# Kernel optimization log

Hardware: AMD Instinct MI355X
Metric: run time of the kernel (lower is better)

## Reference

```python
import jax, jax.numpy as jnp
import numpy as np
import math

B, L, D_MODEL = 4, 2048, 32
H, F = 2, 16  # num_heads, feature_dim (== head_dim)
RD = math.sqrt(F)          # sqrt(input_dim) = 4
R2 = math.sqrt(2.0)
RRD = math.sqrt(RD)        # = 2


def setup_inputs() -> dict:
    key = jax.random.key(0)
    ks = jax.random.split(key, 5)
    s = 1.0 / math.sqrt(D_MODEL)
    return {
        "hidden_states": jax.random.normal(ks[0], (B, L, D_MODEL), jnp.float32),
        "Wq": jax.random.normal(ks[1], (D_MODEL, H * F), jnp.float32) * s,
        "Wk": jax.random.normal(ks[2], (D_MODEL, H * F), jnp.float32) * s,
        "Wv": jax.random.normal(ks[3], (D_MODEL, H * F), jnp.float32) * s,
        "Wo": jax.random.normal(ks[4], (H * F, D_MODEL), jnp.float32) * s,
    }


def _lin_attn(Q, K, V):
    # Q,K,V: [b,h,n,d] with d=f=e=16. Taylor-series linear attention, causal.
    b, h, n, d = Q.shape
    # 2nd-order term
    A2 = jnp.cumsum(jnp.einsum('bhnd,bhnf,bhne->bhndef', K, V, K), axis=2) / (RD * R2)
    Q2 = jnp.einsum('bhnd,bhne->bhnde', Q, Q) / (RD * R2)
    T2 = jnp.einsum('bhnde,bhndef->bhnf', Q2, A2)
    # 1st-order term
    A1 = jnp.cumsum(jnp.einsum('bhnd,bhne->bhnde', K, V), axis=2) / RRD
    T1 = jnp.einsum('bhnd,bhnde->bhne', Q / RRD, A1)
    # 0th-order term
    T0 = jnp.cumsum(V, axis=2)
    # denominators
    K2cs = jnp.cumsum(jnp.einsum('bhnd,bhne->bhnde', K, K), axis=2) / (RD * R2)
    D2 = jnp.einsum('bhnde,bhnde->bhn', Q2, K2cs)
    D1 = jnp.einsum('bhnd,bhnd->bhn', Q, jnp.cumsum(K, axis=2)) / (RRD ** 2)
    D0 = jnp.broadcast_to(jnp.arange(1, n + 1, dtype=Q.dtype), (b, h, n))
    numerator = T0 + T1 + T2
    denominator = D0 + D1 + D2
    return numerator / denominator[..., None]  # [b,h,n,f]


def reference(hidden_states, Wq, Wk, Wv, Wo):
    b, l, _ = hidden_states.shape
    q = (hidden_states @ Wq).reshape(b, l, H, F).transpose(0, 2, 1, 3)
    k = (hidden_states @ Wk).reshape(b, l, H, F).transpose(0, 2, 1, 3)
    v = (hidden_states @ Wv).reshape(b, l, H, F).transpose(0, 2, 1, 3)
    y = _lin_attn(q, k, v)                       # [b,h,l,f]
    y = y.transpose(0, 2, 1, 3).reshape(b, l, H * F)  # b l (h d)
    return y @ Wo
```

## Files before the change

kernel.cpp:

```cpp
#include <hip/hip_runtime.h>

#define L_SEQ 2048
#define NH 2
#define FD 16
#define BH 8
#define NQT 16
#define NSC 16

typedef _Float16 half4f __attribute__((ext_vector_type(4)));
typedef float floatx4 __attribute__((ext_vector_type(4)));

struct FalseT { static constexpr bool value = false; };
struct TrueT  { static constexpr bool value = true;  };

__global__ __launch_bounds__(256) void qkv_proj_kernel(
    const float* __restrict__ hs, const float* __restrict__ Wq,
    const float* __restrict__ Wk, const float* __restrict__ Wv,
    _Float16* __restrict__ q, _Float16* __restrict__ k,
    _Float16* __restrict__ v) {
  __shared__ float sW[3][32][32];
  __shared__ float sH[32][32];
  int tid = threadIdx.x;
  float* swf = &sW[0][0][0];
  for (int i = tid; i < 3072; i += 256)
    swf[i] = (i < 1024) ? Wq[i] : (i < 2048) ? Wk[i - 1024] : Wv[i - 2048];
  int row0 = blockIdx.x * 32;
  int r0 = tid >> 5, c = tid & 31;
  for (int p = 0; p < 4; p++) {
    int r = r0 + p * 8;
    sH[r][c] = hs[(size_t)(row0 + r) * 32 + c];
  }
  __syncthreads();
  int hh = c >> 4, f = c & 15;
  for (int p = 0; p < 4; p++) {
    int r = r0 + p * 8;
    float aq = 0.f, ak = 0.f, av = 0.f;
#pragma unroll
    for (int i = 0; i < 32; i++) {
      float h = sH[r][i];
      aq += h * sW[0][i][c];
      ak += h * sW[1][i][c];
      av += h * sW[2][i][c];
    }
    int row = row0 + r;
    int b = row >> 11, l = row & (L_SEQ - 1);
    size_t idx = (((size_t)(b * NH + hh)) * L_SEQ + l) * FD + f;
    q[idx] = (_Float16)(aq * 0.25f);
    k[idx] = (_Float16)ak;
    v[idx] = (_Float16)av;
  }
}

__global__ __launch_bounds__(256) void attn_partial_kernel(
    const _Float16* __restrict__ q, const _Float16* __restrict__ k,
    const _Float16* __restrict__ v, float* __restrict__ pnum,
    float* __restrict__ pden) {
  __shared__ _Float16 sK[128][24];
  __shared__ _Float16 sVT[16][136];
  int tid = threadIdx.x;
  int bh = blockIdx.y;
  int x = blockIdx.x;
  int qt = 0;
  while ((qt + 1) * (qt + 2) / 2 <= x) qt++;
  int sc = x - qt * (qt + 1) / 2;

  {
    int s = tid >> 1, h = tid & 1;
    const _Float16* kp = k + ((size_t)bh * L_SEQ + sc * 128 + s) * FD + 8 * h;
    const _Float16* vp = v + ((size_t)bh * L_SEQ + sc * 128 + s) * FD + 8 * h;
    uint4 kw = *(const uint4*)kp;
    *(uint4*)&sK[s][8 * h] = kw;
    union { uint4 u; _Float16 e[8]; } vu;
    vu.u = *(const uint4*)vp;
#pragma unroll
    for (int i = 0; i < 8; i++) sVT[8 * h + i][s] = vu.e[i];
  }

  int lane = tid & 63;
  int wid = tid >> 6;
  int lm = lane & 15, lg = lane >> 4;

  half4f qf[2];
  {
    const _Float16* qb = q + ((size_t)bh * L_SEQ + qt * 128 + wid * 32) * FD;
#pragma unroll
    for (int sub = 0; sub < 2; sub++)
      qf[sub] = *(const half4f*)(qb + (sub * 16 + lm) * FD + 4 * lg);
  }
  floatx4 o[2];
  float dn[2];
#pragma unroll
  for (int i = 0; i < 2; i++) {
    o[i] = (floatx4){0.f, 0.f, 0.f, 0.f};
    dn[i] = 0.f;
  }
  int tq[2];
#pragma unroll
  for (int sub = 0; sub < 2; sub++)
    tq[sub] = qt * 128 + wid * 32 + sub * 16 + lm;
  int sb = sc * 128 + 4 * lg;

  __syncthreads();

  auto body = [&](auto mc) {
    constexpr bool MASK = decltype(mc)::value;
#pragma unroll
    for (int st = 0; st < 8; st++) {
      half4f kf = *(const half4f*)&sK[st * 16 + lm][4 * lg];
      half4f vf = *(const half4f*)&sVT[lm][st * 16 + 4 * lg];
#pragma unroll
      for (int sub = 0; sub < 2; sub++) {
        floatx4 sT = __builtin_amdgcn_mfma_f32_16x16x16f16(
            kf, qf[sub], (floatx4){0.f, 0.f, 0.f, 0.f}, 0, 0, 0);
        float wvv[4];
#pragma unroll
        for (int r = 0; r < 4; r++) {
          float a = sT[r];
          float wr = (0.5f * a + 1.f) * a + 1.f;
          if (MASK) wr = (sb + st * 16 + r <= tq[sub]) ? wr : 0.f;
          wvv[r] = wr;
          dn[sub] += wr;
        }
        half4f wf = {(_Float16)wvv[0], (_Float16)wvv[1],
                     (_Float16)wvv[2], (_Float16)wvv[3]};
        o[sub] = __builtin_amdgcn_mfma_f32_16x16x16f16(wf, vf, o[sub], 0, 0, 0);
      }
    }
  };
  if (sc < qt) body(FalseT{}); else body(TrueT{});

#pragma unroll
  for (int sub = 0; sub < 2; sub++) {
    dn[sub] += __shfl_xor(dn[sub], 16, 64);
    dn[sub] += __shfl_xor(dn[sub], 32, 64);
  }

  size_t pb = ((size_t)(bh * NQT + qt) * NSC + sc) * 128;
  float* nb = pnum + (pb + wid * 32) * 16;
#pragma unroll
  for (int sub = 0; sub < 2; sub++)
#pragma unroll
    for (int r = 0; r < 4; r++)
      nb[(sub * 16 + 4 * lg + r) * 16 + lm] = o[sub][r];
  if (lg == 0) {
#pragma unroll
    for (int sub = 0; sub < 2; sub++)
      pden[pb + wid * 32 + sub * 16 + lm] = dn[sub];
  }
}

__global__ __launch_bounds__(256) void reduce_outproj_kernel(
    const float* __restrict__ pnum, const float* __restrict__ pden,
    const float* __restrict__ Wo, float* __restrict__ out) {
  __shared__ float sY[64][33];
  __shared__ float sWo[32][32];
  int tid = threadIdx.x;
  for (int i = tid; i < 1024; i += 256) (&sWo[0][0])[i] = Wo[i];

  int ql = tid >> 2, fq = tid & 3;
  int t = blockIdx.x * 64 + ql;
  int b = blockIdx.y;
  int qt = t >> 7;
  int qloc = t & 127;

  for (int h = 0; h < NH; h++) {
    int bh = b * NH + h;
    size_t tb = ((size_t)(bh * NQT + qt) * NSC) * 128;
    const float* nb = pnum + (tb + qloc) * 16 + fq * 4;
    const float* db = pden + tb + qloc;
    float a0 = 0.f, a1 = 0.f, a2 = 0.f, a3 = 0.f, den = 0.f;
    for (int sc = 0; sc <= qt; sc++) {
      float4 p = *(const float4*)(nb + (size_t)sc * 128 * 16);
      a0 += p.x; a1 += p.y; a2 += p.z; a3 += p.w;
      den += db[(size_t)sc * 128];
    }
    float inv = 1.f / den;
    int cb = h * 16 + fq * 4;
    sY[ql][cb + 0] = a0 * inv;
    sY[ql][cb + 1] = a1 * inv;
    sY[ql][cb + 2] = a2 * inv;
    sY[ql][cb + 3] = a3 * inv;
  }
  __syncthreads();

  int c = tid & 31, r0 = tid >> 5;
  float wo[32];
#pragma unroll
  for (int i = 0; i < 32; i++) wo[i] = sWo[i][c];
#pragma unroll
  for (int p = 0; p < 8; p++) {
    int r = r0 + p * 8;
    float a = 0.f;
#pragma unroll
    for (int i = 0; i < 32; i++) a += sY[r][i] * wo[i];
    out[((size_t)b * L_SEQ + blockIdx.x * 64 + r) * 32 + c] = a;
  }
}

extern "C" void kernel_launch(void* const* d_in, const int* in_sizes, int n_in,
                              void* d_out, int out_size, void* d_ws, size_t ws_size,
                              hipStream_t stream) {
  const float* hs = (const float*)d_in[0];
  const float* Wq = (const float*)d_in[1];
  const float* Wk = (const float*)d_in[2];
  const float* Wv = (const float*)d_in[3];
  const float* Wo = (const float*)d_in[4];
  float* out = (float*)d_out;

  char* wb = (char*)d_ws;
  const size_t PER = (size_t)BH * L_SEQ * FD;
  _Float16* qh = (_Float16*)wb;
  _Float16* kh = qh + PER;
  _Float16* vh = kh + PER;
  float* pnum = (float*)(wb + 3 * PER * sizeof(_Float16));
  float* pden = pnum + (size_t)BH * NQT * NSC * 128 * 16;

  qkv_proj_kernel<<<256, 256, 0, stream>>>(hs, Wq, Wk, Wv, qh, kh, vh);
  attn_partial_kernel<<<dim3(136, BH), 256, 0, stream>>>(qh, kh, vh, pnum, pden);
  reduce_outproj_kernel<<<dim3(32, 4), 256, 0, stream>>>(pnum, pden, Wo, out);
}
```

Baseline: 90.07 us.

## Fuse attention, reduction and output projection into one per-query-tile kernel

Replaces the split-KV partial kernel and the separate reduce/out-projection kernel with a single kernel. Each block owns a 32-query tile for both heads of one batch and loops serially over all causal 128-key chunks, then normalizes and applies Wo in place. This removes the partial numerator/denominator round-trip through global memory and one launch. In exchange, per-block work is serial and unbalanced, the longest tile walks all 16 chunks, and only 256 blocks run, with processing ordered longest-first.

```diff
diff --git a/kernel.cpp b/kernel.cpp
--- a/kernel.cpp
+++ b/kernel.cpp
@@ -4,8 +4,9 @@
 #define NH 2
 #define FD 16
 #define BH 8
-#define NQT 16
-#define NSC 16
+#define QT 32
+#define NT 64
+#define SCW 128
 
 typedef _Float16 half4f __attribute__((ext_vector_type(4)));
 typedef float floatx4 __attribute__((ext_vector_type(4)));
@@ -51,135 +52,86 @@
   }
 }
 
-__global__ __launch_bounds__(256) void attn_partial_kernel(
+__global__ __launch_bounds__(256) void attn_fused_kernel(
     const _Float16* __restrict__ q, const _Float16* __restrict__ k,
-    const _Float16* __restrict__ v, float* __restrict__ pnum,
-    float* __restrict__ pden) {
-  __shared__ _Float16 sK[128][24];
-  __shared__ _Float16 sVT[16][136];
+    const _Float16* __restrict__ v, const float* __restrict__ Wo,
+    float* __restrict__ out) {
+  __shared__ _Float16 sK[NH][128][24];
+  __shared__ _Float16 sVT[NH][16][136];
+  __shared__ float sDen[4][16];
+  __shared__ float sY[QT][33];
+  __shared__ float sWo[32][32];
+
   int tid = threadIdx.x;
-  int bh = blockIdx.y;
-  int x = blockIdx.x;
-  int qt = 0;
-  while ((qt + 1) * (qt + 2) / 2 <= x) qt++;
-  int sc = x - qt * (qt + 1) / 2;
-
-  {
-    int s = tid >> 1, h = tid & 1;
-    const _Float16* kp = k + ((size_t)bh * L_SEQ + sc * 128 + s) * FD + 8 * h;
-    const _Float16* vp = v + ((size_t)bh * L_SEQ + sc * 128 + s) * FD + 8 * h;
-    uint4 kw = *(const uint4*)kp;
-    *(uint4*)&sK[s][8 * h] = kw;
-    union { uint4 u; _Float16 e[8]; } vu;
-    vu.u = *(const uint4*)vp;
-#pragma unroll
-    for (int i = 0; i < 8; i++) sVT[8 * h + i][s] = vu.e[i];
-  }
-
+  int b = blockIdx.y;
+  int t = NT - 1 - (int)blockIdx.x;
   int lane = tid & 63;
   int wid = tid >> 6;
   int lm = lane & 15, lg = lane >> 4;
+  int h = wid >> 1, sub = wid & 1;
+  int bh = b * NH + h;
 
-  half4f qf[2];
-  {
-    const _Float16* qb = q + ((size_t)bh * L_SEQ + qt * 128 + wid * 32) * FD;
-#pragma unroll
-    for (int sub = 0; sub < 2; sub++)
-      qf[sub] = *(const half4f*)(qb + (sub * 16 + lm) * FD + 4 * lg);
-  }
-  floatx4 o[2];
-  float dn[2];
-#pragma unroll
-  for (int i = 0; i < 2; i++) {
-    o[i] = (floatx4){0.f, 0.f, 0.f, 0.f};
-    dn[i] = 0.f;
-  }
-  int tq[2];
-#pragma unroll
-  for (int sub = 0; sub < 2; sub++)
-    tq[sub] = qt * 128 + wid * 32 + sub * 16 + lm;
-  int sb = sc * 128 + 4 * lg;
+  for (int i = tid; i < 1024; i += 256) (&sWo[0][0])[i] = Wo[i];
 
-  __syncthreads();
+  int q0 = t * QT + sub * 16;
+  half4f qf = *(const half4f*)(q + ((size_t)bh * L_SEQ + q0 + lm) * FD + 4 * lg);
 
-  auto body = [&](auto mc) {
+  floatx4 o = (floatx4){0.f, 0.f, 0.f, 0.f};
+  float dn = 0.f;
+  int tq = q0 + lm;
+  int lastc = t >> 2;
+  int ss = tid >> 1, hf = tid & 1;
+
+  auto body = [&](int sc, auto mc) {
     constexpr bool MASK = decltype(mc)::value;
+    int sb = sc * SCW + 4 * lg;
 #pragma unroll
     for (int st = 0; st < 8; st++) {
-      half4f kf = *(const half4f*)&sK[st * 16 + lm][4 * lg];
-      half4f vf = *(const half4f*)&sVT[lm][st * 16 + 4 * lg];
+      half4f kf = *(const half4f*)&sK[h][st * 16 + lm][4 * lg];
+      half4f vf = *(const half4f*)&sVT[h][lm][st * 16 + 4 * lg];
+      floatx4 sT = __builtin_amdgcn_mfma_f32_16x16x16f16(
+          kf, qf, (floatx4){0.f, 0.f, 0.f, 0.f}, 0, 0, 0);
+      float wvv[4];
 #pragma unroll
-      for (int sub = 0; sub < 2; sub++) {
-        floatx4 sT = __builtin_amdgcn_mfma_f32_16x16x16f16(
-            kf, qf[sub], (floatx4){0.f, 0.f, 0.f, 0.f}, 0, 0, 0);
-        float wvv[4];
-#pragma unroll
-        for (int r = 0; r < 4; r++) {
-          float a = sT[r];
-          float wr = (0.5f * a + 1.f) * a + 1.f;
-          if (MASK) wr = (sb + st * 16 + r <= tq[sub]) ? wr : 0.f;
-          wvv[r] = wr;
-          dn[sub] += wr;
-        }
-        half4f wf = {(_Float16)wvv[0], (_Float16)wvv[1],
-                     (_Float16)wvv[2], (_Float16)wvv[3]};
-        o[sub] = __builtin_amdgcn_mfma_f32_16x16x16f16(wf, vf, o[sub], 0, 0, 0);
+      for (int r = 0; r < 4; r++) {
+        float a = sT[r];
+        float wr = (0.5f * a + 1.f) * a + 1.f;
+        if (MASK) wr = (sb + st * 16 + r <= tq) ? wr : 0.f;
+        wvv[r] = wr;
+        dn += wr;
       }
+      half4f wf = {(_Float16)wvv[0], (_Float16)wvv[1],
+                   (_Float16)wvv[2], (_Float16)wvv[3]};
+      o = __builtin_amdgcn_mfma_f32_16x16x16f16(wf, vf, o, 0, 0, 0);
     }
   };
-  if (sc < qt) body(FalseT{}); else body(TrueT{});
 
+  for (int sc = 0; sc <= lastc; sc++) {
+    __syncthreads();
 #pragma unroll
-  for (int sub = 0; sub < 2; sub++) {
-    dn[sub] += __shfl_xor(dn[sub], 16, 64);
-    dn[sub] += __shfl_xor(dn[sub], 32, 64);
+    for (int hh = 0; hh < NH; hh++) {
+      const _Float16* kp =
+          k + (((size_t)(b * NH + hh)) * L_SEQ + sc * SCW + ss) * FD + 8 * hf;
+      const _Float16* vp =
+          v + (((size_t)(b * NH + hh)) * L_SEQ + sc * SCW + ss) * FD + 8 * hf;
+      *(uint4*)&sK[hh][ss][8 * hf] = *(const uint4*)kp;
+      union { uint4 u; _Float16 e[8]; } vu;
+      vu.u = *(const uint4*)vp;
+#pragma unroll
+      for (int i = 0; i < 8; i++) sVT[hh][8 * hf + i][ss] = vu.e[i];
+    }
+    __syncthreads();
+    if (sc < lastc) body(sc, FalseT{}); else body(sc, TrueT{});
   }
 
-  size_t pb = ((size_t)(bh * NQT + qt) * NSC + sc) * 128;
-  float* nb = pnum + (pb + wid * 32) * 16;
+  dn += __shfl_xor(dn, 16, 64);
+  dn += __shfl_xor(dn, 32, 64);
+  if (lg == 0) sDen[wid][lm] = dn;
+  __syncthreads();
 #pragma unroll
-  for (int sub = 0; sub < 2; sub++)
-#pragma unroll
-    for (int r = 0; r < 4; r++)
-      nb[(sub * 16 + 4 * lg + r) * 16 + lm] = o[sub][r];
-  if (lg == 0) {
-#pragma unroll
-    for (int sub = 0; sub < 2; sub++)
-      pden[pb + wid * 32 + sub * 16 + lm] = dn[sub];
-  }
-}
-
-__global__ __launch_bounds__(256) void reduce_outproj_kernel(
-    const float* __restrict__ pnum, const float* __restrict__ pden,
-    const float* __restrict__ Wo, float* __restrict__ out) {
-  __shared__ float sY[64][33];
-  __shared__ float sWo[32][32];
-  int tid = threadIdx.x;
-  for (int i = tid; i < 1024; i += 256) (&sWo[0][0])[i] = Wo[i];
-
-  int ql = tid >> 2, fq = tid & 3;
-  int t = blockIdx.x * 64 + ql;
-  int b = blockIdx.y;
-  int qt = t >> 7;
-  int qloc = t & 127;
-
-  for (int h = 0; h < NH; h++) {
-    int bh = b * NH + h;
-    size_t tb = ((size_t)(bh * NQT + qt) * NSC) * 128;
-    const float* nb = pnum + (tb + qloc) * 16 + fq * 4;
-    const float* db = pden + tb + qloc;
-    float a0 = 0.f, a1 = 0.f, a2 = 0.f, a3 = 0.f, den = 0.f;
-    for (int sc = 0; sc <= qt; sc++) {
-      float4 p = *(const float4*)(nb + (size_t)sc * 128 * 16);
-      a0 += p.x; a1 += p.y; a2 += p.z; a3 += p.w;
-      den += db[(size_t)sc * 128];
-    }
-    float inv = 1.f / den;
-    int cb = h * 16 + fq * 4;
-    sY[ql][cb + 0] = a0 * inv;
-    sY[ql][cb + 1] = a1 * inv;
-    sY[ql][cb + 2] = a2 * inv;
-    sY[ql][cb + 3] = a3 * inv;
+  for (int r = 0; r < 4; r++) {
+    float dd = sDen[wid][4 * lg + r];
+    sY[sub * 16 + 4 * lg + r][h * 16 + lm] = o[r] / dd;
   }
   __syncthreads();
 
@@ -188,12 +140,12 @@
 #pragma unroll
   for (int i = 0; i < 32; i++) wo[i] = sWo[i][c];
 #pragma unroll
-  for (int p = 0; p < 8; p++) {
+  for (int p = 0; p < 4; p++) {
     int r = r0 + p * 8;
     float a = 0.f;
 #pragma unroll
     for (int i = 0; i < 32; i++) a += sY[r][i] * wo[i];
-    out[((size_t)b * L_SEQ + blockIdx.x * 64 + r) * 32 + c] = a;
+    out[((size_t)b * L_SEQ + t * QT + r) * 32 + c] = a;
   }
 }
 
@@ -212,10 +164,7 @@
   _Float16* qh = (_Float16*)wb;
   _Float16* kh = qh + PER;
   _Float16* vh = kh + PER;
-  float* pnum = (float*)(wb + 3 * PER * sizeof(_Float16));
-  float* pden = pnum + (size_t)BH * NQT * NSC * 128 * 16;
 
   qkv_proj_kernel<<<256, 256, 0, stream>>>(hs, Wq, Wk, Wv, qh, kh, vh);
-  attn_partial_kernel<<<dim3(136, BH), 256, 0, stream>>>(qh, kh, vh, pnum, pden);
-  reduce_outproj_kernel<<<dim3(32, 4), 256, 0, stream>>>(pnum, pden, Wo, out);
+  attn_fused_kernel<<<dim3(NT, 4), 256, 0, stream>>>(qh, kh, vh, Wo, out);
 }
```

Measured after the change: 87.77 us. -2.6%, faster.
